# Performance work log

Hardware: AMD Instinct MI355X
Metric: run time of the kernel (lower is better)

## Reference

```python
import jax, jax.numpy as jnp
import numpy as np

EMBED_DIM = 1024
NUM_HEADS = 16
HEAD_DIM = EMBED_DIM // NUM_HEADS


def setup_inputs() -> dict:
    key = jax.random.key(0)
    ks = jax.random.split(key, 12)
    B, S, E = 2, 2048, EMBED_DIM
    scale = 1.0 / np.sqrt(E)
    inp = {
        "query": jax.random.normal(ks[0], (B, S, E), dtype=jnp.float32),
        "key": jax.random.normal(ks[1], (B, S, E), dtype=jnp.float32),
        "value": jax.random.normal(ks[2], (B, S, E), dtype=jnp.float32),
        "key_padding_mask": jax.random.randint(ks[3], (B, S), 0, 2).astype(bool),
        # Linear params (torch nn.Linear: y = x @ W.T + b)
        "Wq": jax.random.normal(ks[4], (E, E), dtype=jnp.float32) * scale,
        "bq": jnp.zeros((E,), dtype=jnp.float32),
        "Wk": jax.random.normal(ks[5], (E, E), dtype=jnp.float32) * scale,
        "bk": jnp.zeros((E,), dtype=jnp.float32),
        "Wv": jax.random.normal(ks[6], (E, E), dtype=jnp.float32) * scale,
        "bv": jnp.zeros((E,), dtype=jnp.float32),
        "Wo": jax.random.normal(ks[7], (E, E), dtype=jnp.float32) * scale,
        "bo": jnp.zeros((E,), dtype=jnp.float32),
    }
    return inp


def reference(query, key, value, key_padding_mask, Wq, bq, Wk, bk, Wv, bv, Wo, bo):
    B, Sq, E = query.shape
    H, D = NUM_HEADS, HEAD_DIM

    def split_heads(x, W, b):
        y = x @ W.T + b                      # [B, S, E]
        return y.reshape(B, -1, H, D).transpose(0, 2, 1, 3)  # [B, H, S, D]

    q = split_heads(query, Wq, bq)
    k = split_heads(key, Wk, bk)
    v = split_heads(value, Wv, bv)

    scores = jnp.einsum("bhqd,bhkd->bhqk", q, k) / jnp.sqrt(jnp.float32(D))
    scores = jnp.where(key_padding_mask[:, None, None, :], -jnp.inf, scores)
    probs = jax.nn.softmax(scores, axis=-1)  # dropout p=0.0 -> identity
    attn = jnp.einsum("bhqk,bhkd->bhqd", probs, v)
    attn = attn.transpose(0, 2, 1, 3).reshape(B, Sq, E)
    return attn @ Wo.T + bo
```

## Files before the change

### kernel.cpp

```cpp
#include <hip/hip_runtime.h>
#include <hip/hip_bf16.h>

#define BATCH 2
#define SEQ   2048
#define EMBED 1024
#define NHEAD 16
#define HDIM  64

typedef __bf16 bf16x8 __attribute__((ext_vector_type(8)));
typedef float  floatx4 __attribute__((ext_vector_type(4)));

__global__ void detect_kernel(const void* qptr, const void* mptr, int* flags) {
    if (threadIdx.x != 0 || blockIdx.x != 0) return;
    const unsigned short* u = (const unsigned short*)qptr;
    int sane = 0;
    for (int i = 0; i < 64; ++i) {
        int e = (u[2 * i] >> 7) & 0xff;
        if (e >= 117 && e <= 137) sane++;
    }
    flags[0] = (sane >= 40) ? 1 : 0;
    const unsigned int* w = (const unsigned int*)mptr;
    int all01 = 1, allf = 1;
    for (int i = 0; i < 64; ++i) {
        unsigned int x = w[i];
        if (!(x == 0u || x == 1u)) all01 = 0;
        if (!(x == 0u || x == 0x3F800000u)) allf = 0;
    }
    flags[1] = (all01 || allf) ? 0 : 1;
}

__global__ void mask_bits(const void* mptr, const int* flags,
                          unsigned long long* mb) {
    const int i = blockIdx.x * 64 + threadIdx.x;
    int v;
    if (flags[1]) v = (((const unsigned char*)mptr)[i] != 0);
    else          v = (((const unsigned int*)mptr)[i] != 0u);
    unsigned long long bal = __ballot(v);
    if (threadIdx.x == 0) mb[blockIdx.x] = bal;
}

struct ConvAll { const void* src[7]; void* dst[7]; unsigned n[7]; };

__global__ __launch_bounds__(256) void convert_all(ConvAll a, const int* flags) {
    if (flags[0]) return;
    const int t = blockIdx.y;
    const unsigned n8 = a.n[t] / 8;
    const unsigned stride = gridDim.x * blockDim.x;
    for (unsigned i = blockIdx.x * blockDim.x + threadIdx.x; i < n8; i += stride) {
        const unsigned base = i * 8;
        const float* s = (const float*)a.src[t] + base;
        __hip_bfloat16 tmp[8];
#pragma unroll
        for (int j = 0; j < 8; ++j) tmp[j] = __float2bfloat16(s[j]);
        *(uint4*)((__hip_bfloat16*)a.dst[t] + base) = *(const uint4*)tmp;
    }
}

__device__ __forceinline__ void gload_lds16(const __hip_bfloat16* g, __bf16* l) {
    __builtin_amdgcn_global_load_lds(
        (const __attribute__((address_space(1))) unsigned int*)g,
        (__attribute__((address_space(3))) unsigned int*)l, 16, 0, 0);
}

struct GemmIO {
    const void* Xr; const __hip_bfloat16* Xc;
    const void* Wr; const __hip_bfloat16* Wc;
    const void* br;
    void* Y;
};
struct GemmArgs { GemmIO io[3]; };

__global__ __launch_bounds__(256, 2) void gemm_mfma(
        GemmArgs args, int M, int N, int K, const int* flags, int omode) {
    const GemmIO io = args.io[blockIdx.z];
    const int isbf = flags[0];
    const __hip_bfloat16* Xp = isbf ? (const __hip_bfloat16*)io.Xr : io.Xc;
    const __hip_bfloat16* Wp = isbf ? (const __hip_bfloat16*)io.Wr : io.Wc;
    __shared__ __bf16 Xs[128 * 64];
    __shared__ __bf16 Ws[128 * 64];
    const int lane = threadIdx.x & 63, wv = threadIdx.x >> 6;
    const int wr = wv >> 1, wc = wv & 1;
    const int l = lane & 15, quad = lane >> 4;
    const int row0 = blockIdx.y * 128, col0 = blockIdx.x * 128;

    const int srow = lane >> 3;
    const int schunk = (lane & 7) ^ srow;
    const __hip_bfloat16* xbase = Xp + (size_t)(row0 + srow) * K + schunk * 8;
    const __hip_bfloat16* wbase = Wp + (size_t)(col0 + srow) * K + schunk * 8;

    floatx4 acc[4][4] = {};

    for (int k0 = 0; k0 < K; k0 += 64) {
        __syncthreads();
#pragma unroll
        for (int i = 0; i < 4; ++i) {
            const int instr = wv * 4 + i;
            gload_lds16(xbase + (size_t)instr * 8 * K + k0, &Xs[instr * 512]);
        }
#pragma unroll
        for (int i = 0; i < 4; ++i) {
            const int instr = wv * 4 + i;
            gload_lds16(wbase + (size_t)instr * 8 * K + k0, &Ws[instr * 512]);
        }
        __syncthreads();
#pragma unroll
        for (int kk = 0; kk < 2; ++kk) {
            bf16x8 af[4], bfr[4];
#pragma unroll
            for (int m = 0; m < 4; ++m)
                af[m] = *(const bf16x8*)
                    &Xs[(wr * 64 + m * 16 + l) * 64 + ((kk * 4 + quad) ^ (l & 7)) * 8];
#pragma unroll
            for (int n = 0; n < 4; ++n)
                bfr[n] = *(const bf16x8*)
                    &Ws[(wc * 64 + n * 16 + l) * 64 + ((kk * 4 + quad) ^ (l & 7)) * 8];
#pragma unroll
            for (int m = 0; m < 4; ++m)
#pragma unroll
                for (int n = 0; n < 4; ++n)
                    acc[m][n] = __builtin_amdgcn_mfma_f32_16x16x32_bf16(
                        af[m], bfr[n], acc[m][n], 0, 0, 0);
        }
    }

#pragma unroll
    for (int m = 0; m < 4; ++m) {
#pragma unroll
        for (int n = 0; n < 4; ++n) {
            const int col = col0 + wc * 64 + n * 16 + l;
            const float bv = isbf
                ? __bfloat162float(((const __hip_bfloat16*)io.br)[col])
                : ((const float*)io.br)[col];
#pragma unroll
            for (int r = 0; r < 4; ++r) {
                const int row = row0 + wr * 64 + m * 16 + quad * 4 + r;
                const float v = acc[m][n][r] + bv;
                if (omode == 0 || isbf)
                    ((__hip_bfloat16*)io.Y)[(size_t)row * N + col] = __float2bfloat16(v);
                else
                    ((float*)io.Y)[(size_t)row * N + col] = v;
            }
        }
    }
}

__global__ __launch_bounds__(256) void transpose_v(
        const __hip_bfloat16* __restrict__ Vp, __hip_bfloat16* __restrict__ Vt) {
    __shared__ __bf16 Ts[64][72];
    const int bh = blockIdx.x, b = bh >> 4, h = bh & 15;
    const int s0 = blockIdx.y * 64;
    const int t = threadIdx.x;
    const int s = t >> 2, c = t & 3;
#pragma unroll
    for (int half = 0; half < 2; ++half) {
        const int cc = c + half * 4;
        bf16x8 v = *(const bf16x8*)(Vp + (size_t)(b * SEQ + s0 + s) * EMBED +
                                    h * HDIM + cc * 8);
#pragma unroll
        for (int j = 0; j < 8; ++j) Ts[cc * 8 + j][s] = v[j];
    }
    __syncthreads();
    const int d = t >> 2;
#pragma unroll
    for (int half = 0; half < 2; ++half) {
        const int cc = c + half * 4;
        bf16x8 v = *(const bf16x8*)&Ts[d][cc * 8];
        *(bf16x8*)(Vt + ((size_t)bh * HDIM + d) * SEQ + s0 + cc * 8) = v;
    }
}

__global__ __launch_bounds__(256) void attn_mfma(
        const __hip_bfloat16* __restrict__ Qb,
        const __hip_bfloat16* __restrict__ Kb,
        const __hip_bfloat16* __restrict__ Vt,
        const unsigned long long* __restrict__ mbits,
        __hip_bfloat16* __restrict__ Ao) {
    const int bh = blockIdx.x, b = bh >> 4, h = bh & 15;
    const int q0 = blockIdx.y * 128;
    const int wv = threadIdx.x >> 6, lane = threadIdx.x & 63;
    const int l = lane & 15, quad = lane >> 4;

    __shared__ __bf16 Ks[128 * 64];
    __shared__ __bf16 Vs[64 * 128];

    bf16x8 aQ[2][2];
#pragma unroll
    for (int g = 0; g < 2; ++g) {
        const int qrow = q0 + wv * 32 + g * 16 + l;
        const __hip_bfloat16* qp =
            Qb + ((size_t)(b * SEQ + qrow)) * EMBED + h * HDIM + quad * 8;
        aQ[g][0] = *(const bf16x8*)qp;
        aQ[g][1] = *(const bf16x8*)(qp + 32);
    }

    floatx4 O[2][4] = {};
    floatx4 Ol[2] = {};
    const float SC2 = 0.125f * 1.44269504088896f;
    const int rho = 8 * (l >> 2) + (l & 3);

    bf16x8 vone;
#pragma unroll
    for (int j = 0; j < 8; ++j) vone[j] = (__bf16)1.0f;

    const int ksrow = lane >> 3, kpc = lane & 7;
    const int vsrow = lane >> 4, vpc = lane & 15;

    for (int k0 = 0; k0 < SEQ; k0 += 128) {
        __syncthreads();
#pragma unroll
        for (int i = 0; i < 4; ++i) {
            const int row = wv * 32 + i * 8 + ksrow;
            const int sc = kpc ^ ((row & 3) | (((row >> 3) & 1) << 2));
            gload_lds16(Kb + ((size_t)(b * SEQ + k0 + row)) * EMBED + h * HDIM +
                            sc * 8,
                        &Ks[(wv * 32 + i * 8) * 64]);
        }
#pragma unroll
        for (int i = 0; i < 4; ++i) {
            const int row = wv * 16 + i * 4 + vsrow;
            const int sc = vpc ^ (row & 15);
            gload_lds16(Vt + ((size_t)(bh * HDIM + row)) * SEQ + k0 + sc * 8,
                        &Vs[(wv * 16 + i * 4) * 128]);
        }
        __syncthreads();

        const unsigned long long mw0 = mbits[b * 32 + (k0 >> 6)];
        const unsigned long long mw1 = mbits[b * 32 + (k0 >> 6) + 1];

#pragma unroll
        for (int kh2 = 0; kh2 < 2; ++kh2) {
            bf16x8 a0[4], a1[4];
#pragma unroll
            for (int n = 0; n < 4; ++n) {
                const int rr = kh2 * 64 + 32 * (n >> 1) + 4 * (n & 1) + rho;
                const int f = (rr & 3) | (((rr >> 3) & 1) << 2);
                a0[n] = *(const bf16x8*)&Ks[rr * 64 + ((quad) ^ f) * 8];
                a1[n] = *(const bf16x8*)&Ks[rr * 64 + ((quad + 4) ^ f) * 8];
            }
            bf16x8 bv[2][4];
#pragma unroll
            for (int kh = 0; kh < 2; ++kh)
#pragma unroll
                for (int dt = 0; dt < 4; ++dt) {
                    const int c = kh2 * 8 + kh * 4 + quad;
                    bv[kh][dt] =
                        *(const bf16x8*)&Vs[(dt * 16 + l) * 128 + (c ^ l) * 8];
                }
            const unsigned long long mw = kh2 ? mw1 : mw0;
            const unsigned mb0 = (unsigned)(mw >> (8 * quad)) & 0xffu;
            const unsigned mb1 = (unsigned)(mw >> (32 + 8 * quad)) & 0xffu;

#pragma unroll
            for (int g = 0; g < 2; ++g) {
                floatx4 S[4];
#pragma unroll
                for (int n = 0; n < 4; ++n) {
                    floatx4 c = {};
                    c = __builtin_amdgcn_mfma_f32_16x16x32_bf16(a0[n], aQ[g][0],
                                                                c, 0, 0, 0);
                    c = __builtin_amdgcn_mfma_f32_16x16x32_bf16(a1[n], aQ[g][1],
                                                                c, 0, 0, 0);
                    S[n] = c;
                }
#pragma unroll
                for (int n = 0; n < 4; ++n) {
                    const unsigned byt = (n < 2) ? mb0 : mb1;
#pragma unroll
                    for (int r = 0; r < 4; ++r) {
                        const float p = exp2f(S[n][r] * SC2);
                        S[n][r] = ((byt >> (4 * (n & 1) + r)) & 1u) ? 0.f : p;
                    }
                }
#pragma unroll
                for (int kh = 0; kh < 2; ++kh) {
                    bf16x8 ap;
#pragma unroll
                    for (int j = 0; j < 4; ++j) {
                        ap[j]     = (__bf16)S[2 * kh][j];
                        ap[j + 4] = (__bf16)S[2 * kh + 1][j];
                    }
#pragma unroll
                    for (int dt = 0; dt < 4; ++dt)
                        O[g][dt] = __builtin_amdgcn_mfma_f32_16x16x32_bf16(
                            ap, bv[kh][dt], O[g][dt], 0, 0, 0);
                    Ol[g] = __builtin_amdgcn_mfma_f32_16x16x32_bf16(
                        ap, vone, Ol[g], 0, 0, 0);
                }
            }
        }
    }
#pragma unroll
    for (int g = 0; g < 2; ++g)
#pragma unroll
        for (int r = 0; r < 4; ++r) {
            const float lr = Ol[g][r];
            const float inv = (lr > 0.f) ? (1.f / lr) : 0.f;
            const int row = q0 + wv * 32 + g * 16 + quad * 4 + r;
#pragma unroll
            for (int dt = 0; dt < 4; ++dt)
                Ao[((size_t)(b * SEQ + row)) * EMBED + h * HDIM + dt * 16 + l] =
                    __float2bfloat16(O[g][dt][r] * inv);
        }
}

extern "C" void kernel_launch(void* const* d_in, const int* in_sizes, int n_in,
                              void* d_out, int out_size, void* d_ws, size_t ws_size,
                              hipStream_t stream) {
    const void* query = d_in[0];
    const void* key   = d_in[1];
    const void* value = d_in[2];
    const void* mask  = d_in[3];

    char* ws = (char*)d_ws;
    int* flags = (int*)ws;
    unsigned long long* mbits = (unsigned long long*)(ws + 1024);
    const size_t TEN = (size_t)BATCH * SEQ * EMBED;
    const size_t WEL = (size_t)EMBED * EMBED;
    char* p = ws + 32768;
    __hip_bfloat16* Qc  = (__hip_bfloat16*)p;  p += TEN * 2;
    __hip_bfloat16* Kc  = (__hip_bfloat16*)p;  p += TEN * 2;
    __hip_bfloat16* Vc  = (__hip_bfloat16*)p;  p += TEN * 2;
    __hip_bfloat16* Wqc = (__hip_bfloat16*)p;  p += WEL * 2;
    __hip_bfloat16* Wkc = (__hip_bfloat16*)p;  p += WEL * 2;
    __hip_bfloat16* Wvc = (__hip_bfloat16*)p;  p += WEL * 2;
    __hip_bfloat16* Woc = (__hip_bfloat16*)p;  p += WEL * 2;
    __hip_bfloat16* Qb  = (__hip_bfloat16*)p;  p += TEN * 2;
    __hip_bfloat16* Kb  = (__hip_bfloat16*)p;  p += TEN * 2;
    __hip_bfloat16* Vp  = (__hip_bfloat16*)p;  p += TEN * 2;
    __hip_bfloat16* Ao  = Qc;
    __hip_bfloat16* Vt  = Kc;

    const int M = BATCH * SEQ;

    detect_kernel<<<1, 64, 0, stream>>>(query, mask, flags);

    ConvAll ca;
    ca.src[0] = query;    ca.dst[0] = Qc;  ca.n[0] = (unsigned)TEN;
    ca.src[1] = key;      ca.dst[1] = Kc;  ca.n[1] = (unsigned)TEN;
    ca.src[2] = value;    ca.dst[2] = Vc;  ca.n[2] = (unsigned)TEN;
    ca.src[3] = d_in[4];  ca.dst[3] = Wqc; ca.n[3] = (unsigned)WEL;
    ca.src[4] = d_in[6];  ca.dst[4] = Wkc; ca.n[4] = (unsigned)WEL;
    ca.src[5] = d_in[8];  ca.dst[5] = Wvc; ca.n[5] = (unsigned)WEL;
    ca.src[6] = d_in[10]; ca.dst[6] = Woc; ca.n[6] = (unsigned)WEL;
    convert_all<<<dim3(256, 7), 256, 0, stream>>>(ca, flags);

    mask_bits<<<BATCH * SEQ / 64, 64, 0, stream>>>(mask, flags, mbits);

    GemmArgs qkv;
    qkv.io[0] = { query, Qc, d_in[4],  Wqc, d_in[5],  (void*)Qb };
    qkv.io[1] = { key,   Kc, d_in[6],  Wkc, d_in[7],  (void*)Kb };
    qkv.io[2] = { value, Vc, d_in[8],  Wvc, d_in[9],  (void*)Vp };
    gemm_mfma<<<dim3(EMBED / 128, M / 128, 3), 256, 0, stream>>>(
        qkv, M, EMBED, EMBED, flags, 0);

    transpose_v<<<dim3(BATCH * NHEAD, SEQ / 64), 256, 0, stream>>>(Vp, Vt);

    attn_mfma<<<dim3(BATCH * NHEAD, SEQ / 128), 256, 0, stream>>>(Qb, Kb, Vt,
                                                                  mbits, Ao);

    GemmArgs og;
    og.io[0] = { Ao, Ao, d_in[10], Woc, d_in[11], d_out };
    og.io[1] = og.io[0];
    og.io[2] = og.io[0];
    gemm_mfma<<<dim3(EMBED / 128, M / 128, 1), 256, 0, stream>>>(
        og, M, EMBED, EMBED, flags, 1);
}
```

Measured before the change: 263.4 us.

## Double-buffer attention K/V tiles, fold softmax scale into Q, move masking into V

```diff
diff --git a/kernel.cpp b/kernel.cpp
--- a/kernel.cpp
+++ b/kernel.cpp
@@ -10,15 +10,8 @@
 typedef __bf16 bf16x8 __attribute__((ext_vector_type(8)));
 typedef float  floatx4 __attribute__((ext_vector_type(4)));
 
-__global__ void detect_kernel(const void* qptr, const void* mptr, int* flags) {
-    if (threadIdx.x != 0 || blockIdx.x != 0) return;
-    const unsigned short* u = (const unsigned short*)qptr;
-    int sane = 0;
-    for (int i = 0; i < 64; ++i) {
-        int e = (u[2 * i] >> 7) & 0xff;
-        if (e >= 117 && e <= 137) sane++;
-    }
-    flags[0] = (sane >= 40) ? 1 : 0;
+__global__ void mask_flags_bits(const void* qptr, const void* mptr,
+                                unsigned long long* mb, int* flags) {
     const unsigned int* w = (const unsigned int*)mptr;
     int all01 = 1, allf = 1;
     for (int i = 0; i < 64; ++i) {
@@ -26,17 +19,23 @@
         if (!(x == 0u || x == 1u)) all01 = 0;
         if (!(x == 0u || x == 0x3F800000u)) allf = 0;
     }
-    flags[1] = (all01 || allf) ? 0 : 1;
-}
-
-__global__ void mask_bits(const void* mptr, const int* flags,
-                          unsigned long long* mb) {
+    const int bytemask = (all01 || allf) ? 0 : 1;
     const int i = blockIdx.x * 64 + threadIdx.x;
     int v;
-    if (flags[1]) v = (((const unsigned char*)mptr)[i] != 0);
+    if (bytemask) v = (((const unsigned char*)mptr)[i] != 0);
     else          v = (((const unsigned int*)mptr)[i] != 0u);
     unsigned long long bal = __ballot(v);
     if (threadIdx.x == 0) mb[blockIdx.x] = bal;
+    if (blockIdx.x == 0 && threadIdx.x == 0) {
+        const unsigned short* u = (const unsigned short*)qptr;
+        int sane = 0;
+        for (int k = 0; k < 64; ++k) {
+            int e = (u[2 * k] >> 7) & 0xff;
+            if (e >= 117 && e <= 137) sane++;
+        }
+        flags[0] = (sane >= 40) ? 1 : 0;
+        flags[1] = bytemask;
+    }
 }
 
 struct ConvAll { const void* src[7]; void* dst[7]; unsigned n[7]; };
@@ -67,6 +66,7 @@
     const void* Wr; const __hip_bfloat16* Wc;
     const void* br;
     void* Y;
+    float osc;
 };
 struct GemmArgs { GemmIO io[3]; };
 
@@ -134,7 +134,7 @@
 #pragma unroll
             for (int r = 0; r < 4; ++r) {
                 const int row = row0 + wr * 64 + m * 16 + quad * 4 + r;
-                const float v = acc[m][n][r] + bv;
+                const float v = (acc[m][n][r] + bv) * io.osc;
                 if (omode == 0 || isbf)
                     ((__hip_bfloat16*)io.Y)[(size_t)row * N + col] = __float2bfloat16(v);
                 else
@@ -144,11 +144,89 @@
     }
 }
 
+__global__ __launch_bounds__(256, 2) void gemm_out(
+        const __hip_bfloat16* __restrict__ X,
+        const void* __restrict__ Wr, const __hip_bfloat16* __restrict__ Wc,
+        const void* __restrict__ bias, void* __restrict__ Y,
+        const int* flags) {
+    const int N = EMBED, K = EMBED;
+    const int isbf = flags[0];
+    const __hip_bfloat16* Wp = isbf ? (const __hip_bfloat16*)Wr : Wc;
+    __shared__ __bf16 Xs[64 * 64];
+    __shared__ __bf16 Ws[128 * 64];
+    const int lane = threadIdx.x & 63, wv = threadIdx.x >> 6;
+    const int wr = wv >> 1, wc = wv & 1;
+    const int l = lane & 15, quad = lane >> 4;
+    const int row0 = blockIdx.y * 64, col0 = blockIdx.x * 128;
+
+    const int srow = lane >> 3;
+    const int schunk = (lane & 7) ^ srow;
+    const __hip_bfloat16* xbase = X + (size_t)(row0 + srow) * K + schunk * 8;
+    const __hip_bfloat16* wbase = Wp + (size_t)(col0 + srow) * K + schunk * 8;
+
+    floatx4 acc[2][4] = {};
+
+    for (int k0 = 0; k0 < K; k0 += 64) {
+        __syncthreads();
+#pragma unroll
+        for (int i = 0; i < 2; ++i) {
+            const int instr = wv * 2 + i;
+            gload_lds16(xbase + (size_t)instr * 8 * K + k0, &Xs[instr * 512]);
+        }
+#pragma unroll
+        for (int i = 0; i < 4; ++i) {
+            const int instr = wv * 4 + i;
+            gload_lds16(wbase + (size_t)instr * 8 * K + k0, &Ws[instr * 512]);
+        }
+        __syncthreads();
+#pragma unroll
+        for (int kk = 0; kk < 2; ++kk) {
+            bf16x8 af[2], bfr[4];
+#pragma unroll
+            for (int m = 0; m < 2; ++m)
+                af[m] = *(const bf16x8*)
+                    &Xs[(wr * 32 + m * 16 + l) * 64 + ((kk * 4 + quad) ^ (l & 7)) * 8];
+#pragma unroll
+            for (int n = 0; n < 4; ++n)
+                bfr[n] = *(const bf16x8*)
+                    &Ws[(wc * 64 + n * 16 + l) * 64 + ((kk * 4 + quad) ^ (l & 7)) * 8];
+#pragma unroll
+            for (int m = 0; m < 2; ++m)
+#pragma unroll
+                for (int n = 0; n < 4; ++n)
+                    acc[m][n] = __builtin_amdgcn_mfma_f32_16x16x32_bf16(
+                        af[m], bfr[n], acc[m][n], 0, 0, 0);
+        }
+    }
+
+#pragma unroll
+    for (int m = 0; m < 2; ++m) {
+#pragma unroll
+        for (int n = 0; n < 4; ++n) {
+            const int col = col0 + wc * 64 + n * 16 + l;
+            const float bv = isbf
+                ? __bfloat162float(((const __hip_bfloat16*)bias)[col])
+                : ((const float*)bias)[col];
+#pragma unroll
+            for (int r = 0; r < 4; ++r) {
+                const int row = row0 + wr * 32 + m * 16 + quad * 4 + r;
+                const float v = acc[m][n][r] + bv;
+                if (isbf)
+                    ((__hip_bfloat16*)Y)[(size_t)row * N + col] = __float2bfloat16(v);
+                else
+                    ((float*)Y)[(size_t)row * N + col] = v;
+            }
+        }
+    }
+}
+
 __global__ __launch_bounds__(256) void transpose_v(
-        const __hip_bfloat16* __restrict__ Vp, __hip_bfloat16* __restrict__ Vt) {
+        const __hip_bfloat16* __restrict__ Vp, __hip_bfloat16* __restrict__ Vt,
+        const unsigned long long* __restrict__ mbits) {
     __shared__ __bf16 Ts[64][72];
     const int bh = blockIdx.x, b = bh >> 4, h = bh & 15;
     const int s0 = blockIdx.y * 64;
+    const unsigned long long mw = mbits[b * 32 + blockIdx.y];
     const int t = threadIdx.x;
     const int s = t >> 2, c = t & 3;
 #pragma unroll
@@ -165,6 +243,9 @@
     for (int half = 0; half < 2; ++half) {
         const int cc = c + half * 4;
         bf16x8 v = *(const bf16x8*)&Ts[d][cc * 8];
+#pragma unroll
+        for (int j = 0; j < 8; ++j)
+            if ((mw >> (cc * 8 + j)) & 1ull) v[j] = (__bf16)0.f;
         *(bf16x8*)(Vt + ((size_t)bh * HDIM + d) * SEQ + s0 + cc * 8) = v;
     }
 }
@@ -180,8 +261,8 @@
     const int wv = threadIdx.x >> 6, lane = threadIdx.x & 63;
     const int l = lane & 15, quad = lane >> 4;
 
-    __shared__ __bf16 Ks[128 * 64];
-    __shared__ __bf16 Vs[64 * 128];
+    __shared__ __bf16 Ks[2][128 * 64];
+    __shared__ __bf16 Vs[2][64 * 128];
 
     bf16x8 aQ[2][2];
 #pragma unroll
@@ -195,34 +276,36 @@
 
     floatx4 O[2][4] = {};
     floatx4 Ol[2] = {};
-    const float SC2 = 0.125f * 1.44269504088896f;
     const int rho = 8 * (l >> 2) + (l & 3);
-
-    bf16x8 vone;
-#pragma unroll
-    for (int j = 0; j < 8; ++j) vone[j] = (__bf16)1.0f;
 
     const int ksrow = lane >> 3, kpc = lane & 7;
     const int vsrow = lane >> 4, vpc = lane & 15;
 
-    for (int k0 = 0; k0 < SEQ; k0 += 128) {
-        __syncthreads();
+    auto stage = [&](int k0, int buf) {
 #pragma unroll
         for (int i = 0; i < 4; ++i) {
             const int row = wv * 32 + i * 8 + ksrow;
             const int sc = kpc ^ ((row & 3) | (((row >> 3) & 1) << 2));
             gload_lds16(Kb + ((size_t)(b * SEQ + k0 + row)) * EMBED + h * HDIM +
                             sc * 8,
-                        &Ks[(wv * 32 + i * 8) * 64]);
+                        &Ks[buf][(wv * 32 + i * 8) * 64]);
         }
 #pragma unroll
         for (int i = 0; i < 4; ++i) {
             const int row = wv * 16 + i * 4 + vsrow;
             const int sc = vpc ^ (row & 15);
             gload_lds16(Vt + ((size_t)(bh * HDIM + row)) * SEQ + k0 + sc * 8,
-                        &Vs[(wv * 16 + i * 4) * 128]);
-        }
+                        &Vs[buf][(wv * 16 + i * 4) * 128]);
+        }
+    };
+
+    stage(0, 0);
+    const int NT = SEQ / 128;
+    for (int t = 0; t < NT; ++t) {
         __syncthreads();
+        if (t + 1 < NT) stage((t + 1) * 128, (t + 1) & 1);
+        const int buf = t & 1;
+        const int k0 = t * 128;
 
         const unsigned long long mw0 = mbits[b * 32 + (k0 >> 6)];
         const unsigned long long mw1 = mbits[b * 32 + (k0 >> 6) + 1];
@@ -234,8 +317,8 @@
             for (int n = 0; n < 4; ++n) {
                 const int rr = kh2 * 64 + 32 * (n >> 1) + 4 * (n & 1) + rho;
                 const int f = (rr & 3) | (((rr >> 3) & 1) << 2);
-                a0[n] = *(const bf16x8*)&Ks[rr * 64 + ((quad) ^ f) * 8];
-                a1[n] = *(const bf16x8*)&Ks[rr * 64 + ((quad + 4) ^ f) * 8];
+                a0[n] = *(const bf16x8*)&Ks[buf][rr * 64 + ((quad) ^ f) * 8];
+                a1[n] = *(const bf16x8*)&Ks[buf][rr * 64 + ((quad + 4) ^ f) * 8];
             }
             bf16x8 bv[2][4];
 #pragma unroll
@@ -243,12 +326,18 @@
 #pragma unroll
                 for (int dt = 0; dt < 4; ++dt) {
                     const int c = kh2 * 8 + kh * 4 + quad;
-                    bv[kh][dt] =
-                        *(const bf16x8*)&Vs[(dt * 16 + l) * 128 + (c ^ l) * 8];
+                    bv[kh][dt] = *(const bf16x8*)
+                        &Vs[buf][(dt * 16 + l) * 128 + (c ^ l) * 8];
                 }
             const unsigned long long mw = kh2 ? mw1 : mw0;
-            const unsigned mb0 = (unsigned)(mw >> (8 * quad)) & 0xffu;
-            const unsigned mb1 = (unsigned)(mw >> (32 + 8 * quad)) & 0xffu;
+            bf16x8 vm[2];
+#pragma unroll
+            for (int kh = 0; kh < 2; ++kh)
+#pragma unroll
+                for (int j = 0; j < 8; ++j) {
+                    const int bit = kh * 32 + quad * 8 + j;
+                    vm[kh][j] = ((mw >> bit) & 1ull) ? (__bf16)0.f : (__bf16)1.0f;
+                }
 
 #pragma unroll
             for (int g = 0; g < 2; ++g) {
@@ -263,14 +352,9 @@
                     S[n] = c;
                 }
 #pragma unroll
-                for (int n = 0; n < 4; ++n) {
-                    const unsigned byt = (n < 2) ? mb0 : mb1;
-#pragma unroll
-                    for (int r = 0; r < 4; ++r) {
-                        const float p = exp2f(S[n][r] * SC2);
-                        S[n][r] = ((byt >> (4 * (n & 1) + r)) & 1u) ? 0.f : p;
-                    }
-                }
+                for (int n = 0; n < 4; ++n)
+#pragma unroll
+                    for (int r = 0; r < 4; ++r) S[n][r] = exp2f(S[n][r]);
 #pragma unroll
                 for (int kh = 0; kh < 2; ++kh) {
                     bf16x8 ap;
@@ -284,7 +368,7 @@
                         O[g][dt] = __builtin_amdgcn_mfma_f32_16x16x32_bf16(
                             ap, bv[kh][dt], O[g][dt], 0, 0, 0);
                     Ol[g] = __builtin_amdgcn_mfma_f32_16x16x32_bf16(
-                        ap, vone, Ol[g], 0, 0, 0);
+                        ap, vm[kh], Ol[g], 0, 0, 0);
                 }
             }
         }
@@ -331,8 +415,9 @@
     __hip_bfloat16* Vt  = Kc;
 
     const int M = BATCH * SEQ;
-
-    detect_kernel<<<1, 64, 0, stream>>>(query, mask, flags);
+    const float QSCALE = 0.125f * 1.44269504088896f;
+
+    mask_flags_bits<<<M / 64, 64, 0, stream>>>(query, mask, mbits, flags);
 
     ConvAll ca;
     ca.src[0] = query;    ca.dst[0] = Qc;  ca.n[0] = (unsigned)TEN;
@@ -342,26 +427,20 @@
     ca.src[4] = d_in[6];  ca.dst[4] = Wkc; ca.n[4] = (unsigned)WEL;
     ca.src[5] = d_in[8];  ca.dst[5] = Wvc; ca.n[5] = (unsigned)WEL;
     ca.src[6] = d_in[10]; ca.dst[6] = Woc; ca.n[6] = (unsigned)WEL;
-    convert_all<<<dim3(256, 7), 256, 0, stream>>>(ca, flags);
-
-    mask_bits<<<BATCH * SEQ / 64, 64, 0, stream>>>(mask, flags, mbits);
+    convert_all<<<dim3(64, 7), 256, 0, stream>>>(ca, flags);
 
     GemmArgs qkv;
-    qkv.io[0] = { query, Qc, d_in[4],  Wqc, d_in[5],  (void*)Qb };
-    qkv.io[1] = { key,   Kc, d_in[6],  Wkc, d_in[7],  (void*)Kb };
-    qkv.io[2] = { value, Vc, d_in[8],  Wvc, d_in[9],  (void*)Vp };
+    qkv.io[0] = { query, Qc, d_in[4],  Wqc, d_in[5],  (void*)Qb, QSCALE };
+    qkv.io[1] = { key,   Kc, d_in[6],  Wkc, d_in[7],  (void*)Kb, 1.0f };
+    qkv.io[2] = { value, Vc, d_in[8],  Wvc, d_in[9],  (void*)Vp, 1.0f };
     gemm_mfma<<<dim3(EMBED / 128, M / 128, 3), 256, 0, stream>>>(
         qkv, M, EMBED, EMBED, flags, 0);
 
-    transpose_v<<<dim3(BATCH * NHEAD, SEQ / 64), 256, 0, stream>>>(Vp, Vt);
-
-    attn_mfma<<<dim3(BATCH * NHEAD, SEQ / 128), 256, 0, stream>>>(Qb, Kb, Vt,
-                                                                  mbits, Ao);
-
-    GemmArgs og;
-    og.io[0] = { Ao, Ao, d_in[10], Woc, d_in[11], d_out };
-    og.io[1] = og.io[0];
-    og.io[2] = og.io[0];
-    gemm_mfma<<<dim3(EMBED / 128, M / 128, 1), 256, 0, stream>>>(
-        og, M, EMBED, EMBED, flags, 1);
-}
+    transpose_v<<<dim3(BATCH * NHEAD, SEQ / 64), 256, 0, stream>>>(Vp, Vt, mbits);
+
+    attn_mfma<<<dim3(BATCH * NHEAD, SEQ / 128), 256, 0, stream>>>(
+        Qb, Kb, Vt, mbits, Ao);
+
+    gemm_out<<<dim3(EMBED / 128, M / 64), 256, 0, stream>>>(
+        Ao, d_in[10], Woc, d_in[11], d_out, flags);
+}
```

Result: faster. 254.8 us (-3.3%).
